# Performance work log

Measured on AMD Instinct MI355X. Metric: run time of the kernel, lower is better.

The kernel has to match this reference:

```python
import jax, jax.numpy as jnp
import numpy as np

NUM_EMBEDDINGS = 1024
EMBED_DIM = 256
EMA_DECAY = 0.99
EPS = 1e-05


def setup_inputs() -> dict:
    key = jax.random.key(0)
    k1, k2, k3 = jax.random.split(key, 3)
    B, D, H, W = 32, EMBED_DIM, 32, 32
    z = jax.random.normal(k1, (B, D, H, W), dtype=jnp.float32)
    # torch init: uniform(-1/K, 1/K)
    scale = 1.0 / NUM_EMBEDDINGS
    embedding = jax.random.uniform(k2, (NUM_EMBEDDINGS, EMBED_DIM), dtype=jnp.float32,
                                   minval=-scale, maxval=scale)
    ema_cluster_size = jnp.zeros((NUM_EMBEDDINGS,), dtype=jnp.float32)
    # buffer initialized to a copy of the embedding weights
    ema_embed_sum = embedding.copy()
    return {"z": z, "embedding": embedding,
            "ema_cluster_size": ema_cluster_size, "ema_embed_sum": ema_embed_sum}


def reference(z, embedding, ema_cluster_size, ema_embed_sum):
    B, D, H, W = z.shape
    K = embedding.shape[0]
    # (B, D, H, W) -> (N, D) with N = B*H*W
    z_flat = jnp.transpose(z, (0, 2, 3, 1)).reshape(-1, D)
    # squared L2 distances: ||z||^2 - 2 z E^T + ||e||^2  -> (N, K)
    distances = (jnp.sum(z_flat * z_flat, axis=1, keepdims=True)
                 - 2.0 * z_flat @ embedding.T
                 + jnp.sum(embedding * embedding, axis=1)[None, :])
    indices = jnp.argmin(distances, axis=1)  # (N,) int32
    z_q = embedding[indices].reshape(B, H, W, D).transpose(0, 3, 1, 2)  # (B, D, H, W)

    # training-mode EMA updates (pure functional: return new buffers / codebook)
    ones = jnp.ones((z_flat.shape[0],), dtype=z_flat.dtype)
    counts = jax.ops.segment_sum(ones, indices, num_segments=K)          # (K,)
    embed_sum = jax.ops.segment_sum(z_flat, indices, num_segments=K)     # (K, D)
    new_cs = EMA_DECAY * ema_cluster_size + (1.0 - EMA_DECAY) * counts
    new_es = EMA_DECAY * ema_embed_sum + (1.0 - EMA_DECAY) * embed_sum
    n = jnp.sum(new_cs)
    cluster_size = (new_cs + EPS) / (n + K * EPS) * n
    new_embedding = new_es / cluster_size[:, None]

    # commitment loss and straight-through estimator
    commitment_loss = jnp.mean((z - jax.lax.stop_gradient(z_q)) ** 2)
    z_q_st = z + jax.lax.stop_gradient(z_q - z)
    indices_grid = indices.reshape(B, H, W)
    return (z_q_st, commitment_loss, indices_grid, new_embedding, new_cs, new_es)
```

## Files before the change

kernel.cpp:

```cpp
#include <hip/hip_runtime.h>

#define D_  256
#define K_  1024
#define HW_ 1024
#define N_  32768

#define WS_COUNTS  262144
#define WS_EMBSUM  266240
#define WS_LOSS    1314816
#define WS_NSUM    1314820
#define WS_ENMAX   1314824
#define WS_ZERO0   262144
#define WS_ZEROLEN 1052684
#define WS_NEWCS   1314828
#define WS_ENORM   1318924
#define WS_E16     1454096
#define WS_TOTAL   1978384

#define O_ZQ   0
#define O_LOSS 8388608
#define O_IDX  8388609
#define O_EMB  8421377
#define O_NCS  8683521
#define O_NES  8684545

typedef unsigned short u16;
typedef _Float16 f16x8 __attribute__((ext_vector_type(8)));
typedef float f32x4 __attribute__((ext_vector_type(4)));

__device__ __forceinline__ unsigned f16x2pack(float a, float b) {
  union { _Float16 h; unsigned short u; } ca, cb;
  ca.h = (_Float16)a; cb.h = (_Float16)b;
  return (unsigned)ca.u | ((unsigned)cb.u << 16);
}

__device__ __forceinline__ float pw256_sq(const float* __restrict__ p, int stride) {
  float tot0 = 0.f, tot1 = 0.f;
#pragma unroll
  for (int h = 0; h < 2; ++h) {
    const float* q = p + h * 128 * stride;
    float r[8];
#pragma unroll
    for (int j = 0; j < 8; ++j) { float x = q[j * stride]; r[j] = __fmul_rn(x, x); }
    for (int i = 8; i < 128; i += 8)
#pragma unroll
      for (int j = 0; j < 8; ++j) {
        float x = q[(i + j) * stride];
        r[j] = __fadd_rn(r[j], __fmul_rn(x, x));
      }
    float s = __fadd_rn(__fadd_rn(__fadd_rn(r[0], r[1]), __fadd_rn(r[2], r[3])),
                        __fadd_rn(__fadd_rn(r[4], r[5]), __fadd_rn(r[6], r[7])));
    if (h == 0) tot0 = s; else tot1 = s;
  }
  return __fadd_rn(tot0, tot1);
}

__global__ void vq_eprep(const float* __restrict__ E, float* __restrict__ enorm,
                         u16* __restrict__ E16, unsigned* __restrict__ enmax) {
  int gid = blockIdx.x * 256 + threadIdx.x;
  if (gid < K_) {
    float v = pw256_sq(E + gid * D_, 1);
    enorm[gid] = v;
    atomicMax(enmax, __float_as_uint(v));
  }
  unsigned* E16w = (unsigned*)E16;
  for (int wd = gid; wd < (K_ * D_ / 2); wd += 8192) {
    float2 x = *(const float2*)(E + 2 * wd);
    E16w[wd] = f16x2pack(512.0f * x.x, 512.0f * x.y);
  }
}

template <int CTRL>
__device__ __forceinline__ float dppmin(float v) {
  int p = __builtin_amdgcn_update_dpp(0, __float_as_int(v), CTRL, 0xF, 0xF, true);
  return fminf(v, __int_as_float(p));
}

__device__ __forceinline__ void exact_update(
    const float* zrow, const float* __restrict__ E, int t, int c,
    const float* zn_s, const float* en_s, unsigned long long* best_s) {
  const float* ep = E + c * D_;
  float a = 0.f;
  for (int d0 = 0; d0 < 256; d0 += 8) {
    f32x4 z0 = *(const f32x4*)(zrow + d0);
    f32x4 z1 = *(const f32x4*)(zrow + d0 + 4);
    float4 e0 = *(const float4*)(ep + d0);
    float4 e1 = *(const float4*)(ep + d0 + 4);
    a = __fmaf_rn(z0[0], e0.x, a); a = __fmaf_rn(z0[1], e0.y, a);
    a = __fmaf_rn(z0[2], e0.z, a); a = __fmaf_rn(z0[3], e0.w, a);
    a = __fmaf_rn(z1[0], e1.x, a); a = __fmaf_rn(z1[1], e1.y, a);
    a = __fmaf_rn(z1[2], e1.z, a); a = __fmaf_rn(z1[3], e1.w, a);
  }
  float s = __fadd_rn(__fsub_rn(zn_s[t], __fmul_rn(2.0f, a)), en_s[c]);
  unsigned long long key = ((unsigned long long)__float_as_uint(s) << 32) | (unsigned)c;
  atomicMin(&best_s[t], key);
}

#define TCAP 96
#define ZP  260

__global__ __launch_bounds__(256, 4) void vq_main(
    const float* __restrict__ z, const float* __restrict__ E,
    const u16* __restrict__ E16, const float* __restrict__ enorm,
    const unsigned* __restrict__ enmax,
    float* __restrict__ embsum, float* __restrict__ loss_sum,
    float* __restrict__ counts, float* __restrict__ out_zq,
    float* __restrict__ out_idx) {
  __shared__ __align__(16) float zs[32 * ZP];
  __shared__ float en_s[K_];
  __shared__ float zn_s[32];
  __shared__ float mg_s[32];
  __shared__ unsigned rmin_s[32];
  __shared__ unsigned long long best_s[32];
  __shared__ unsigned tcount[4];
  __shared__ unsigned tlist[4][TCAP];
  __shared__ float wred[4];

  const int tid = threadIdx.x;
  const int tile = blockIdx.x;
  const int bimg = tile >> 5;
  const int hw0 = (tile & 31) << 5;
  const float* zb = z + bimg * (D_ * HW_) + hw0;
  const int n0 = bimg * HW_ + hw0;

#pragma unroll
  for (int r = 0; r < 8; ++r) {
    int ii = r * 256 + tid;
    int d = ii >> 3, t4 = (ii & 7) * 4;
    float4 v = *(const float4*)(zb + d * HW_ + t4);
    zs[(t4 + 0) * ZP + d] = v.x; zs[(t4 + 1) * ZP + d] = v.y;
    zs[(t4 + 2) * ZP + d] = v.z; zs[(t4 + 3) * ZP + d] = v.w;
  }
  for (int i = tid; i < K_; i += 256) en_s[i] = enorm[i];
  if (tid < 4) tcount[tid] = 0;
  __syncthreads();
  if (tid < 32) {
    float zn = pw256_sq(&zs[tid * ZP], 1);
    zn_s[tid] = zn;
    float em = __uint_as_float(*enmax);
    mg_s[tid] = 0.00390625f * sqrtf(zn * em) + 5e-4f;
    rmin_s[tid] = 0xFFFFFFFFu;
    best_s[tid] = ~0ull;
  }
  __syncthreads();

  const int lane = tid & 63;
  const int w = tid >> 6;
  const int l15 = lane & 15, g = lane >> 4;
  const int cw = w * 256;
  const u16* Eb = E16 + (unsigned)(cw + l15) * D_ + g * 8;

  f16x8 efA[2], efB[2];
#pragma unroll
  for (int n = 0; n < 2; ++n)
    efA[n] = *(const f16x8*)(Eb + n * 16 * D_);

  f32x4 acc[2][2];

#define MSTEP(S, EFU, EFF, SN)                                                   \
  {                                                                              \
    const int kk_ = (S) & 7;                                                     \
    {                                                                            \
      const int cn_ = (SN) >> 3, kn_ = (SN) & 7;                                 \
      _Pragma("unroll")                                                          \
      for (int n = 0; n < 2; ++n)                                                \
        EFF[n] = *(const f16x8*)(Eb + (cn_ * 32 + n * 16) * D_ + kn_ * 32);      \
    }                                                                            \
    f16x8 zf_[2];                                                                \
    _Pragma("unroll")                                                            \
    for (int m = 0; m < 2; ++m) {                                                \
      const float* zr = zs + (m * 16 + l15) * ZP + kk_ * 32 + g * 8;             \
      f32x4 lo = *(const f32x4*)zr;                                              \
      f32x4 hi = *(const f32x4*)(zr + 4);                                        \
      f16x8 zc;                                                                  \
      _Pragma("unroll")                                                          \
      for (int j = 0; j < 4; ++j) {                                              \
        zc[j] = (_Float16)lo[j]; zc[4 + j] = (_Float16)hi[j];                    \
      }                                                                          \
      zf_[m] = zc;                                                               \
    }                                                                            \
    _Pragma("unroll")                                                            \
    for (int m = 0; m < 2; ++m)                                                  \
      _Pragma("unroll")                                                          \
      for (int n = 0; n < 2; ++n)                                                \
        acc[m][n] = __builtin_amdgcn_mfma_f32_16x16x32_f16(zf_[m], EFU[n],       \
                                                           acc[m][n], 0, 0, 0);  \
  }

  for (int s2 = 0; s2 < 64; s2 += 2) {
    if ((s2 & 7) == 0) {
      f32x4 z4 = {0.f, 0.f, 0.f, 0.f};
#pragma unroll
      for (int m = 0; m < 2; ++m)
#pragma unroll
        for (int n = 0; n < 2; ++n) acc[m][n] = z4;
    }
    MSTEP(s2, efA, efB, s2 + 1)
    MSTEP(s2 + 1, efB, efA, (s2 + 2) & 63)
    if ((s2 & 7) == 6) {
      const int cb = cw + (s2 >> 3) * 32;
      float enc[2];
#pragma unroll
      for (int n = 0; n < 2; ++n) enc[n] = en_s[cb + n * 16 + l15];
#pragma unroll
      for (int m = 0; m < 2; ++m)
#pragma unroll
        for (int n = 0; n < 2; ++n)
#pragma unroll
          for (int r = 0; r < 4; ++r)
            acc[m][n][r] = __builtin_fmaf(-0.00390625f, acc[m][n][r], enc[n]);
#pragma unroll
      for (int m = 0; m < 2; ++m)
#pragma unroll
        for (int r = 0; r < 4; ++r) {
          float v = fminf(acc[m][0][r], acc[m][1][r]);
          v = dppmin<0xB1>(v);
          v = dppmin<0x4E>(v);
          v = dppmin<0x141>(v);
          v = dppmin<0x140>(v);
          if (l15 == 0) atomicMin(&rmin_s[m * 16 + g * 4 + r], __float_as_uint(v + 4.0f));
        }
#pragma unroll
      for (int m = 0; m < 2; ++m)
#pragma unroll
        for (int r = 0; r < 4; ++r) {
          int t = m * 16 + g * 4 + r;
          float thr = (__uint_as_float(rmin_s[t]) - 4.0f) + mg_s[t];
#pragma unroll
          for (int n = 0; n < 2; ++n) {
            if (acc[m][n][r] <= thr) {
              unsigned pos = atomicAdd(&tcount[w], 1u);
              if (pos < TCAP)
                tlist[w][pos] = ((unsigned)t << 16) | (unsigned)(cb + n * 16 + l15);
            }
          }
        }
    }
  }
#undef MSTEP

  {
    unsigned cnt = tcount[w];
    if (cnt <= TCAP) {
      for (unsigned basei = 0; basei < cnt; basei += 64) {
        unsigned i = basei + (unsigned)lane;
        if (i < cnt) {
          unsigned e = tlist[w][i];
          int t = (int)(e >> 16), c = (int)(e & 1023u);
          exact_update(&zs[t * ZP], E, t, c, zn_s, en_s, best_s);
        }
      }
    } else {
      for (unsigned i = (unsigned)lane; i < 32u * 256u; i += 64) {
        int t = (int)(i >> 8), c = cw + (int)(i & 255u);
        exact_update(&zs[t * ZP], E, t, c, zn_s, en_s, best_s);
      }
    }
  }
  __syncthreads();

  if (tid < 32) {
    int k = (int)(best_s[tid] & 1023ull);
    out_idx[n0 + tid] = (float)k;
    atomicAdd(&counts[k], 1.0f);
  }
  float lsum = 0.f;
  for (int tt = 0; tt < 8; ++tt) {
    int t = w * 8 + tt;
    int k = (int)(best_s[t] & 1023ull);
    const float* Er = E + k * D_;
    float* es = embsum + k * D_;
#pragma unroll
    for (int i = 0; i < 4; ++i) {
      int d = i * 64 + lane;
      float e = Er[d];
      float zv = zs[t * ZP + d];
      float df = __fsub_rn(zv, e);
      lsum += df * df;
      zs[t * ZP + d] = __fadd_rn(zv, __fsub_rn(e, zv));
      atomicAdd(es + d, zv);
    }
  }
#pragma unroll
  for (int o = 32; o > 0; o >>= 1) lsum += __shfl_down(lsum, o, 64);
  if (lane == 0) wred[w] = lsum;
  __syncthreads();
  if (tid == 0) atomicAdd(loss_sum, wred[0] + wred[1] + wred[2] + wred[3]);

  float* ob = out_zq + bimg * (D_ * HW_) + hw0;
#pragma unroll 4
  for (int r = 0; r < 32; ++r) {
    int d = r * 8 + (tid >> 5);
    int t = tid & 31;
    ob[d * HW_ + t] = zs[t * ZP + d];
  }
}

__global__ void vq_newcs_v7(const float* __restrict__ cs_in, const float* __restrict__ counts,
                            float* __restrict__ newcs, float* __restrict__ nsum,
                            const float* __restrict__ loss_sum,
                            float* __restrict__ out_loss, float* __restrict__ out_ncs) {
  int k = blockIdx.x * 256 + threadIdx.x;
  float v = __fadd_rn(__fmul_rn(0.99f, cs_in[k]), __fmul_rn(0.01f, counts[k]));
  newcs[k] = v;
  out_ncs[k] = v;
  float s = v;
#pragma unroll
  for (int o = 32; o > 0; o >>= 1) s += __shfl_down(s, o, 64);
  __shared__ float w[4];
  if ((threadIdx.x & 63) == 0) w[threadIdx.x >> 6] = s;
  __syncthreads();
  if (threadIdx.x == 0) atomicAdd(nsum, w[0] + w[1] + w[2] + w[3]);
  if (k == 0) out_loss[0] = loss_sum[0] * (1.0f / 8388608.0f);
}

__global__ void vq_newemb_v7(const float* __restrict__ es_in, const float* __restrict__ embsum,
                             const float* __restrict__ newcs, const float* __restrict__ nsum,
                             float* __restrict__ out_emb, float* __restrict__ out_nes) {
  int k = blockIdx.x, d = threadIdx.x;
  float n = *nsum;
  float cs = (newcs[k] + 1e-5f) / (n + 1024.0f * 1e-5f) * n;
  float es = __fadd_rn(__fmul_rn(0.99f, es_in[k * D_ + d]),
                       __fmul_rn(0.01f, embsum[k * D_ + d]));
  out_nes[k * D_ + d] = es;
  out_emb[k * D_ + d] = es / cs;
}

extern "C" void kernel_launch(void* const* d_in, const int* in_sizes, int n_in,
                              void* d_out, int out_size, void* d_ws, size_t ws_size,
                              hipStream_t stream) {
  (void)in_sizes; (void)n_in; (void)out_size; (void)ws_size;
  const float* z       = (const float*)d_in[0];
  const float* E       = (const float*)d_in[1];
  const float* ema_cs  = (const float*)d_in[2];
  const float* ema_es  = (const float*)d_in[3];
  float* out = (float*)d_out;
  char* ws = (char*)d_ws;
  float* counts = (float*)(ws + WS_COUNTS);
  float* embsum = (float*)(ws + WS_EMBSUM);
  float* loss_s = (float*)(ws + WS_LOSS);
  float* nsum   = (float*)(ws + WS_NSUM);
  unsigned* enmax = (unsigned*)(ws + WS_ENMAX);
  float* newcs  = (float*)(ws + WS_NEWCS);
  float* enorm  = (float*)(ws + WS_ENORM);
  u16*   e16    = (u16*)(ws + WS_E16);

  hipMemsetAsync(ws + WS_ZERO0, 0, WS_ZEROLEN, stream);
  vq_eprep<<<dim3(32), dim3(256), 0, stream>>>(E, enorm, e16, enmax);
  vq_main<<<dim3(1024), dim3(256), 0, stream>>>(z, E, e16, enorm, enmax,
                                                embsum, loss_s, counts,
                                                out + O_ZQ, out + O_IDX);
  vq_newcs_v7<<<dim3(4), dim3(256), 0, stream>>>(ema_cs, counts, newcs, nsum, loss_s,
                                                 out + O_LOSS, out + O_NCS);
  vq_newemb_v7<<<dim3(K_), dim3(256), 0, stream>>>(ema_es, embsum, newcs, nsum,
                                                   out + O_EMB, out + O_NES);
}
```

Baseline: 215.2 us.

## Fold memset into eprep, compute enorm max per block, merge finalize kernels

Replaces the hipMemsetAsync with zeroing inside the eprep kernel. It drops the global atomicMax for the codebook norm maximum and instead reduces the max per block in vq_main from the enorm values already loaded into shared memory. It also merges the two finalize kernels into one, where each block recomputes the total new cluster size. The aim is to remove two launches and a memset, in exchange for redundant reductions in every block of both vq_main and the finalize kernel.

```diff
diff --git a/kernel.cpp b/kernel.cpp
--- a/kernel.cpp
+++ b/kernel.cpp
@@ -9,10 +9,6 @@
 #define WS_EMBSUM  266240
 #define WS_LOSS    1314816
 #define WS_NSUM    1314820
-#define WS_ENMAX   1314824
-#define WS_ZERO0   262144
-#define WS_ZEROLEN 1052684
-#define WS_NEWCS   1314828
 #define WS_ENORM   1318924
 #define WS_E16     1454096
 #define WS_TOTAL   1978384
@@ -56,18 +52,21 @@
 }
 
 __global__ void vq_eprep(const float* __restrict__ E, float* __restrict__ enorm,
-                         u16* __restrict__ E16, unsigned* __restrict__ enmax) {
+                         u16* __restrict__ E16, float* __restrict__ zero0) {
   int gid = blockIdx.x * 256 + threadIdx.x;
   if (gid < K_) {
     float v = pw256_sq(E + gid * D_, 1);
     enorm[gid] = v;
-    atomicMax(enmax, __float_as_uint(v));
   }
   unsigned* E16w = (unsigned*)E16;
   for (int wd = gid; wd < (K_ * D_ / 2); wd += 8192) {
     float2 x = *(const float2*)(E + 2 * wd);
     E16w[wd] = f16x2pack(512.0f * x.x, 512.0f * x.y);
   }
+  float4 z4 = {0.f, 0.f, 0.f, 0.f};
+  float4* zp = (float4*)zero0;
+  for (int i = gid; i < 65792; i += 8192) zp[i] = z4;
+  if (gid == 0) { zero0[263168] = 0.f; zero0[263169] = 0.f; }
 }
 
 template <int CTRL>
@@ -102,7 +101,6 @@
 __global__ __launch_bounds__(256, 4) void vq_main(
     const float* __restrict__ z, const float* __restrict__ E,
     const u16* __restrict__ E16, const float* __restrict__ enorm,
-    const unsigned* __restrict__ enmax,
     float* __restrict__ embsum, float* __restrict__ loss_sum,
     float* __restrict__ counts, float* __restrict__ out_zq,
     float* __restrict__ out_idx) {
@@ -131,13 +129,23 @@
     zs[(t4 + 0) * ZP + d] = v.x; zs[(t4 + 1) * ZP + d] = v.y;
     zs[(t4 + 2) * ZP + d] = v.z; zs[(t4 + 3) * ZP + d] = v.w;
   }
-  for (int i = tid; i < K_; i += 256) en_s[i] = enorm[i];
+  {
+    float emx = 0.f;
+    for (int i = tid; i < K_; i += 256) {
+      float v = enorm[i];
+      en_s[i] = v;
+      emx = fmaxf(emx, v);
+    }
+#pragma unroll
+    for (int o = 32; o > 0; o >>= 1) emx = fmaxf(emx, __shfl_down(emx, o, 64));
+    if ((tid & 63) == 0) wred[tid >> 6] = emx;
+  }
   if (tid < 4) tcount[tid] = 0;
   __syncthreads();
   if (tid < 32) {
     float zn = pw256_sq(&zs[tid * ZP], 1);
     zn_s[tid] = zn;
-    float em = __uint_as_float(*enmax);
+    float em = fmaxf(fmaxf(wred[0], wred[1]), fmaxf(wred[2], wred[3]));
     mg_s[tid] = 0.00390625f * sqrtf(zn * em) + 5e-4f;
     rmin_s[tid] = 0xFFFFFFFFu;
     best_s[tid] = ~0ull;
@@ -296,30 +304,31 @@
   }
 }
 
-__global__ void vq_newcs_v7(const float* __restrict__ cs_in, const float* __restrict__ counts,
-                            float* __restrict__ newcs, float* __restrict__ nsum,
-                            const float* __restrict__ loss_sum,
-                            float* __restrict__ out_loss, float* __restrict__ out_ncs) {
-  int k = blockIdx.x * 256 + threadIdx.x;
-  float v = __fadd_rn(__fmul_rn(0.99f, cs_in[k]), __fmul_rn(0.01f, counts[k]));
-  newcs[k] = v;
-  out_ncs[k] = v;
-  float s = v;
+__global__ void vq_newfin(const float* __restrict__ cs_in, const float* __restrict__ counts,
+                          const float* __restrict__ es_in, const float* __restrict__ embsum,
+                          const float* __restrict__ loss_sum,
+                          float* __restrict__ out_loss, float* __restrict__ out_ncs,
+                          float* __restrict__ out_emb, float* __restrict__ out_nes) {
+  __shared__ float nred[4];
+  const int k = blockIdx.x, d = threadIdx.x;
+  float s = 0.f;
+  float myv[4];
+#pragma unroll
+  for (int i = 0; i < 4; ++i) {
+    int idx = i * 256 + d;
+    float v = __fadd_rn(__fmul_rn(0.99f, cs_in[idx]), __fmul_rn(0.01f, counts[idx]));
+    myv[i] = v;
+    s += v;
+  }
 #pragma unroll
   for (int o = 32; o > 0; o >>= 1) s += __shfl_down(s, o, 64);
-  __shared__ float w[4];
-  if ((threadIdx.x & 63) == 0) w[threadIdx.x >> 6] = s;
-  __syncthreads();
-  if (threadIdx.x == 0) atomicAdd(nsum, w[0] + w[1] + w[2] + w[3]);
-  if (k == 0) out_loss[0] = loss_sum[0] * (1.0f / 8388608.0f);
-}
-
-__global__ void vq_newemb_v7(const float* __restrict__ es_in, const float* __restrict__ embsum,
-                             const float* __restrict__ newcs, const float* __restrict__ nsum,
-                             float* __restrict__ out_emb, float* __restrict__ out_nes) {
-  int k = blockIdx.x, d = threadIdx.x;
-  float n = *nsum;
-  float cs = (newcs[k] + 1e-5f) / (n + 1024.0f * 1e-5f) * n;
+  if ((d & 63) == 0) nred[d >> 6] = s;
+  __syncthreads();
+  const float n = (nred[0] + nred[1]) + (nred[2] + nred[3]);
+  if (d == (k & 255)) out_ncs[k] = myv[k >> 8];
+  if (k == 0 && d == 0) out_loss[0] = loss_sum[0] * (1.0f / 8388608.0f);
+  float vk = __fadd_rn(__fmul_rn(0.99f, cs_in[k]), __fmul_rn(0.01f, counts[k]));
+  float cs = (vk + 1e-5f) / (n + 1024.0f * 1e-5f) * n;
   float es = __fadd_rn(__fmul_rn(0.99f, es_in[k * D_ + d]),
                        __fmul_rn(0.01f, embsum[k * D_ + d]));
   out_nes[k * D_ + d] = es;
@@ -339,19 +348,14 @@
   float* counts = (float*)(ws + WS_COUNTS);
   float* embsum = (float*)(ws + WS_EMBSUM);
   float* loss_s = (float*)(ws + WS_LOSS);
-  float* nsum   = (float*)(ws + WS_NSUM);
-  unsigned* enmax = (unsigned*)(ws + WS_ENMAX);
-  float* newcs  = (float*)(ws + WS_NEWCS);
   float* enorm  = (float*)(ws + WS_ENORM);
   u16*   e16    = (u16*)(ws + WS_E16);
 
-  hipMemsetAsync(ws + WS_ZERO0, 0, WS_ZEROLEN, stream);
-  vq_eprep<<<dim3(32), dim3(256), 0, stream>>>(E, enorm, e16, enmax);
-  vq_main<<<dim3(1024), dim3(256), 0, stream>>>(z, E, e16, enorm, enmax,
+  vq_eprep<<<dim3(32), dim3(256), 0, stream>>>(E, enorm, e16, counts);
+  vq_main<<<dim3(1024), dim3(256), 0, stream>>>(z, E, e16, enorm,
                                                 embsum, loss_s, counts,
                                                 out + O_ZQ, out + O_IDX);
-  vq_newcs_v7<<<dim3(4), dim3(256), 0, stream>>>(ema_cs, counts, newcs, nsum, loss_s,
-                                                 out + O_LOSS, out + O_NCS);
-  vq_newemb_v7<<<dim3(K_), dim3(256), 0, stream>>>(ema_es, embsum, newcs, nsum,
-                                                   out + O_EMB, out + O_NES);
-}
+  vq_newfin<<<dim3(K_), dim3(256), 0, stream>>>(ema_cs, counts, ema_es, embsum,
+                                                loss_s, out + O_LOSS, out + O_NCS,
+                                                out + O_EMB, out + O_NES);
+}
```

After: 209.5 us. 2.7% less time.
